# Performance work log

Measured on AMD Instinct MI355X. Metric: run time of the kernel, lower is better.

## Reference

```python
import jax, jax.numpy as jnp
import numpy as np

T_STEPS = 64      # AR order p
MAX_T = 65536     # trajectory length
BATCH = 256       # number of sampled trajectories
STD = 0.3


def setup_inputs() -> dict:
    key = jax.random.key(0)
    k1, k2, k3 = jax.random.split(key, 3)
    raw = jax.random.normal(k1, (T_STEPS,), dtype=jnp.float32)
    # torch init: params / sum(|params|)
    params = raw / jnp.sum(jnp.abs(raw))
    bias = jax.random.uniform(k2, (1,), dtype=jnp.float32)
    noise = jax.random.normal(k3, (BATCH, MAX_T), dtype=jnp.float32)
    return {"params": params, "bias": bias, "noise": noise}


def _ar_means(params, bias, length):
    """AR(p) recurrence: mean_i = sum_k params[k] * x[i-1-k] + bias, x init = 0.
    State holds the last p values, most-recent-first (matches the reversed
    indexing inputs[i-1 : i-p-1 : -1] in the torch code)."""
    p = params.shape[0]

    def step(state, _):
        new = jnp.dot(state, params) + bias[0]
        state = jnp.concatenate([new[None], state[:-1]])
        return state, new

    init = jnp.zeros((p,), dtype=params.dtype)
    _, means = jax.lax.scan(step, init, None, length=length)
    return means  # [length]


def reference(params, bias, noise):
    # means of the Normal over the trajectory (deterministic, shared by batch)
    means = _ar_means(params, bias, noise.shape[1])  # [T]
    # reparameterized sample: actions = mean + std * eps, eps ~ N(0, 1)
    actions = means[None, :] + jnp.asarray(STD, noise.dtype) * noise  # [B, T]
    return actions
```

## Files before the change

kernel.cpp:

```cpp
#include <hip/hip_runtime.h>

#define T_LEN   65536
#define BATCH   256
#define P       64
#define K1_LEN  8192
#define K1_THREADS 256
#define DBLK    256

typedef float f4 __attribute__((ext_vector_type(4)));


__global__ __launch_bounds__(K1_THREADS, 1) void ar_k1(const float* __restrict__ params,
                                                       float* __restrict__ R) {
    __shared__ __align__(16) float Rl[K1_LEN];
    __shared__ float p[P];
    __shared__ __align__(16) float Vs[68];
    const int tid = threadIdx.x;
    if (tid < P) p[tid] = params[tid];
    __syncthreads();

    if (tid < 64) {
        float z = 0.f;
        const float pk = p[tid];
        for (int t = 0; t < 64; ++t) {
            float y  = __shfl(z, 0) + 1.0f;
            float zn = __shfl_down(z, 1);
            if (tid == 63) zn = 0.f;
            z = fmaf(pk, y, zn);
            if (tid == 0) Rl[t] = y;
        }
    }
    __syncthreads();

    for (int L = 64; L < K1_LEN; L <<= 1) {
        if (tid <= P) {
            const int j = tid;
            float W0 = 0.f, W1 = 0.f;
            if (j <= P - 1)
                for (int m = 0; m <= P - 1 - j; ++m) W0 = fmaf(p[m + j], Rl[L - 1 - m], W0);
            if (j >= 1)
                for (int m = 0; m <= P - j; ++m) W1 = fmaf(p[m + j - 1], Rl[L - 1 - m], W1);
            Vs[j] = W0 - W1;
        }
        __syncthreads();
        if (tid < 64) {
            const int tau = tid;
            float acc = Rl[tau];
            for (int i = 0; i <= tau; ++i) acc = fmaf(Vs[i], Rl[tau - i], acc);
            Rl[L + tau] = acc;
        }
        {
            const f4* __restrict__ Rl4 = reinterpret_cast<const f4*>(Rl);
            f4* __restrict__ Rl4w = reinterpret_cast<f4*>(Rl);
            const f4* __restrict__ V4 = reinterpret_cast<const f4*>(Vs);
            const int nq = (L - 64) >> 2;
            #pragma unroll 1
            for (int q = tid; q < nq; q += K1_THREADS) {
                f4 w4[17];
                #pragma unroll
                for (int j = 0; j < 17; ++j) w4[j] = Rl4[q + j];
                float a0 = w4[16].x, a1 = w4[16].y, a2 = w4[16].z, a3 = w4[16].w;
                #pragma unroll
                for (int g = 0; g < 16; ++g) {
                    const f4 v  = V4[g];
                    const f4 hi = w4[16 - g];
                    const f4 lo = w4[15 - g];
                    a0 = fmaf(v.x, hi.x, a0); a1 = fmaf(v.x, hi.y, a1);
                    a2 = fmaf(v.x, hi.z, a2); a3 = fmaf(v.x, hi.w, a3);
                    a0 = fmaf(v.y, lo.w, a0); a1 = fmaf(v.y, hi.x, a1);
                    a2 = fmaf(v.y, hi.y, a2); a3 = fmaf(v.y, hi.z, a3);
                    a0 = fmaf(v.z, lo.z, a0); a1 = fmaf(v.z, lo.w, a1);
                    a2 = fmaf(v.z, hi.x, a2); a3 = fmaf(v.z, hi.y, a3);
                    a0 = fmaf(v.w, lo.y, a0); a1 = fmaf(v.w, lo.z, a1);
                    a2 = fmaf(v.w, lo.w, a2); a3 = fmaf(v.w, hi.x, a3);
                }
                const float v64 = Vs[64];
                a0 = fmaf(v64, w4[0].x, a0); a1 = fmaf(v64, w4[0].y, a1);
                a2 = fmaf(v64, w4[0].z, a2); a3 = fmaf(v64, w4[0].w, a3);
                f4 o; o.x = a0; o.y = a1; o.z = a2; o.w = a3;
                Rl4w[((L + 64) >> 2) + q] = o;
            }
        }
        __syncthreads();
    }

    for (int j = tid; j < K1_LEN / 4; j += K1_THREADS)
        reinterpret_cast<f4*>(R)[j] = reinterpret_cast<const f4*>(Rl)[j];
}

__global__ __launch_bounds__(DBLK) void ar_double(const float* __restrict__ params,
                                                  float* __restrict__ R, const int L) {
    __shared__ float p[P];
    __shared__ float tail[P];
    __shared__ float V[P + 1];
    __shared__ float win[DBLK + P];
    const int tid = threadIdx.x;
    const int B0  = blockIdx.x * DBLK;
    if (tid < P) {
        p[tid] = params[tid];
        tail[tid] = R[L - 1 - tid];
    }
    for (int j = tid; j < DBLK + P; j += DBLK) {
        const int g = B0 - P + j;
        win[j] = (g >= 0) ? R[g] : 0.f;
    }
    __syncthreads();
    if (tid <= P) {
        const int j = tid;
        float W0 = 0.f, W1 = 0.f;
        if (j <= P - 1)
            for (int m = 0; m <= P - 1 - j; ++m) W0 = fmaf(p[m + j], tail[m], W0);
        if (j >= 1)
            for (int m = 0; m <= P - j; ++m) W1 = fmaf(p[m + j - 1], tail[m], W1);
        V[j] = W0 - W1;
    }
    __syncthreads();
    float acc = win[P + tid];
    #pragma unroll
    for (int i = 0; i <= P; ++i) acc = fmaf(V[i], win[P + tid - i], acc);
    R[L + B0 + tid] = acc;
}

__global__ __launch_bounds__(256) void ar_out(const float* __restrict__ R,
                                              const float* __restrict__ bias,
                                              const float* __restrict__ noise,
                                              float* __restrict__ out) {
    const int i4 = blockIdx.x * 256 + threadIdx.x;
    const float b = bias[0];
    const int t4 = i4 & (T_LEN / 4 - 1);
    const f4 r4 = reinterpret_cast<const f4*>(R)[t4];
    const f4 n4 = __builtin_nontemporal_load(reinterpret_cast<const f4*>(noise) + i4);
    f4 o;
    o.x = fmaf(0.3f, n4.x, b * r4.x);
    o.y = fmaf(0.3f, n4.y, b * r4.y);
    o.z = fmaf(0.3f, n4.z, b * r4.z);
    o.w = fmaf(0.3f, n4.w, b * r4.w);
    __builtin_nontemporal_store(o, reinterpret_cast<f4*>(out) + i4);
}

extern "C" void kernel_launch(void* const* d_in, const int* in_sizes, int n_in,
                              void* d_out, int out_size, void* d_ws, size_t ws_size,
                              hipStream_t stream) {
    const float* params = (const float*)d_in[0];
    const float* bias   = (const float*)d_in[1];
    const float* noise  = (const float*)d_in[2];
    float* out = (float*)d_out;
    float* R   = (float*)d_ws;

    hipLaunchKernelGGL(ar_k1, dim3(1), dim3(K1_THREADS), 0, stream, params, R);
    for (int L = K1_LEN; L < T_LEN; L <<= 1)
        hipLaunchKernelGGL(ar_double, dim3(L / DBLK), dim3(DBLK), 0, stream,
                           params, R, L);
    hipLaunchKernelGGL(ar_out, dim3((BATCH * (T_LEN / 4)) / 256), dim3(256),
                       0, stream, R, bias, noise, out);
}
```

Before: 175.0 us.

## Parallelize AR doubling weights and fold first global doubling into k1

The V-vector weight computation used to run as a serial 64-term loop in 65 threads. It now runs across all 256 threads, each computing a 16-term partial sum, followed by a small reduction. The params buffer is zero-padded to 128 entries so the partial-sum loops need no bounds checks. The single-block ar_k1 also performs the 8192-to-16384 doubling step itself and writes that step straight to global memory, which removes one ar_double launch. The triangular tau loop is fully unrolled with predicated loads. The cost is an extra barrier per step and some extra zero work.

```diff
diff --git a/kernel.cpp b/kernel.cpp
--- a/kernel.cpp
+++ b/kernel.cpp
@@ -13,10 +13,11 @@
 __global__ __launch_bounds__(K1_THREADS, 1) void ar_k1(const float* __restrict__ params,
                                                        float* __restrict__ R) {
     __shared__ __align__(16) float Rl[K1_LEN];
-    __shared__ float p[P];
+    __shared__ float p[128];
+    __shared__ float Wp[64][4];
     __shared__ __align__(16) float Vs[68];
     const int tid = threadIdx.x;
-    if (tid < P) p[tid] = params[tid];
+    if (tid < 128) p[tid] = (tid < P) ? params[tid] : 0.f;
     __syncthreads();
 
     if (tid < 64) {
@@ -32,26 +33,43 @@
     }
     __syncthreads();
 
-    for (int L = 64; L < K1_LEN; L <<= 1) {
-        if (tid <= P) {
-            const int j = tid;
-            float W0 = 0.f, W1 = 0.f;
-            if (j <= P - 1)
-                for (int m = 0; m <= P - 1 - j; ++m) W0 = fmaf(p[m + j], Rl[L - 1 - m], W0);
-            if (j >= 1)
-                for (int m = 0; m <= P - j; ++m) W1 = fmaf(p[m + j - 1], Rl[L - 1 - m], W1);
-            Vs[j] = W0 - W1;
+    for (int L = 64; L <= K1_LEN; L <<= 1) {
+        const bool last = (L == K1_LEN);
+        {
+            const int j = tid >> 2, c = tid & 3;
+            const int mbase = c << 4;
+            float w = 0.f;
+            #pragma unroll
+            for (int mm = 0; mm < 16; ++mm) {
+                const int m = mbase + mm;
+                w = fmaf(p[m + j], Rl[L - 1 - m], w);
+            }
+            Wp[j][c] = w;
         }
         __syncthreads();
-        if (tid < 64) {
+        if (tid <= P) {
+            const float wj  = (tid < P)
+                ? (Wp[tid][0] + Wp[tid][1] + Wp[tid][2] + Wp[tid][3]) : 0.f;
+            const float wm1 = (tid >= 1)
+                ? (Wp[tid-1][0] + Wp[tid-1][1] + Wp[tid-1][2] + Wp[tid-1][3]) : 0.f;
+            Vs[tid] = wj - wm1;
+        }
+        __syncthreads();
+        if (tid < P) {
             const int tau = tid;
             float acc = Rl[tau];
-            for (int i = 0; i <= tau; ++i) acc = fmaf(Vs[i], Rl[tau - i], acc);
-            Rl[L + tau] = acc;
+            #pragma unroll
+            for (int i = 0; i < P; ++i) {
+                const int idx = (tau - i) > 0 ? (tau - i) : 0;
+                const float v = (i <= tau) ? Vs[i] : 0.f;
+                acc = fmaf(v, Rl[idx], acc);
+            }
+            if (last) R[L + tau] = acc; else Rl[L + tau] = acc;
         }
         {
             const f4* __restrict__ Rl4 = reinterpret_cast<const f4*>(Rl);
             f4* __restrict__ Rl4w = reinterpret_cast<f4*>(Rl);
+            f4* __restrict__ Rg4  = reinterpret_cast<f4*>(R);
             const f4* __restrict__ V4 = reinterpret_cast<const f4*>(Vs);
             const int nq = (L - 64) >> 2;
             #pragma unroll 1
@@ -78,7 +96,8 @@
                 a0 = fmaf(v64, w4[0].x, a0); a1 = fmaf(v64, w4[0].y, a1);
                 a2 = fmaf(v64, w4[0].z, a2); a3 = fmaf(v64, w4[0].w, a3);
                 f4 o; o.x = a0; o.y = a1; o.z = a2; o.w = a3;
-                Rl4w[((L + 64) >> 2) + q] = o;
+                if (last) Rg4[((L + 64) >> 2) + q] = o;
+                else      Rl4w[((L + 64) >> 2) + q] = o;
             }
         }
         __syncthreads();
@@ -90,29 +109,38 @@
 
 __global__ __launch_bounds__(DBLK) void ar_double(const float* __restrict__ params,
                                                   float* __restrict__ R, const int L) {
-    __shared__ float p[P];
-    __shared__ float tail[P];
+    __shared__ float p[128];
+    __shared__ float tl[P];
+    __shared__ float Wp[64][4];
     __shared__ float V[P + 1];
     __shared__ float win[DBLK + P];
     const int tid = threadIdx.x;
     const int B0  = blockIdx.x * DBLK;
-    if (tid < P) {
-        p[tid] = params[tid];
-        tail[tid] = R[L - 1 - tid];
-    }
+    if (tid < 128) p[tid] = (tid < P) ? params[tid] : 0.f;
+    if (tid < P)   tl[tid] = R[L - 1 - tid];
     for (int j = tid; j < DBLK + P; j += DBLK) {
         const int g = B0 - P + j;
         win[j] = (g >= 0) ? R[g] : 0.f;
     }
     __syncthreads();
+    {
+        const int j = tid >> 2, c = tid & 3;
+        const int mbase = c << 4;
+        float w = 0.f;
+        #pragma unroll
+        for (int mm = 0; mm < 16; ++mm) {
+            const int m = mbase + mm;
+            w = fmaf(p[m + j], tl[m], w);
+        }
+        Wp[j][c] = w;
+    }
+    __syncthreads();
     if (tid <= P) {
-        const int j = tid;
-        float W0 = 0.f, W1 = 0.f;
-        if (j <= P - 1)
-            for (int m = 0; m <= P - 1 - j; ++m) W0 = fmaf(p[m + j], tail[m], W0);
-        if (j >= 1)
-            for (int m = 0; m <= P - j; ++m) W1 = fmaf(p[m + j - 1], tail[m], W1);
-        V[j] = W0 - W1;
+        const float wj  = (tid < P)
+            ? (Wp[tid][0] + Wp[tid][1] + Wp[tid][2] + Wp[tid][3]) : 0.f;
+        const float wm1 = (tid >= 1)
+            ? (Wp[tid-1][0] + Wp[tid-1][1] + Wp[tid-1][2] + Wp[tid-1][3]) : 0.f;
+        V[tid] = wj - wm1;
     }
     __syncthreads();
     float acc = win[P + tid];
@@ -148,7 +176,7 @@
     float* R   = (float*)d_ws;
 
     hipLaunchKernelGGL(ar_k1, dim3(1), dim3(K1_THREADS), 0, stream, params, R);
-    for (int L = K1_LEN; L < T_LEN; L <<= 1)
+    for (int L = 2 * K1_LEN; L < T_LEN; L <<= 1)
         hipLaunchKernelGGL(ar_double, dim3(L / DBLK), dim3(DBLK), 0, stream,
                            params, R, L);
     hipLaunchKernelGGL(ar_out, dim3((BATCH * (T_LEN / 4)) / 256), dim3(256),
```

Result: faster. 167.4 us (-4.3%).
